# Optimization experiments

Measured on AMD Instinct MI355X. Metric: run time of the kernel, lower is better.

Reference implementation:

```python
import jax, jax.numpy as jnp
import numpy as np

N_NODES = 50000
N_EDGES = 600000
F_IN = 128   # nfeature
H = 128      # nhidden (must equal nfeature due to original code's gcn2 init)
C = 10       # nclass


def setup_inputs() -> dict:
    key = jax.random.key(0)
    ks = jax.random.split(key, 8)
    row = jax.random.randint(ks[0], (N_EDGES,), 0, N_NODES)
    col = jax.random.randint(ks[1], (N_EDGES,), 0, N_NODES)
    label = jax.random.randint(ks[2], (N_EDGES,), 0, C)
    features = jax.random.normal(ks[3], (N_NODES, F_IN), dtype=jnp.float32)
    s1 = 1.0 / np.sqrt(F_IN)
    W1 = jax.random.uniform(ks[4], (H, F_IN), jnp.float32, -s1, s1)
    b1 = jnp.zeros((H,), jnp.float32)
    s2 = 1.0 / np.sqrt(H)
    W2 = jax.random.uniform(ks[5], (H, H), jnp.float32, -s2, s2)
    b2 = jnp.zeros((H,), jnp.float32)
    s3 = 1.0 / np.sqrt(2 * H)
    Wfc = jax.random.uniform(ks[6], (C, 2 * H), jnp.float32, -s3, s3)
    bfc = jnp.zeros((C,), jnp.float32)
    return {"features": features, "W1": W1, "b1": b1, "W2": W2, "b2": b2,
            "Wfc": Wfc, "bfc": bfc, "row": row, "col": col, "label": label}


def gcn_conv(x, row, col, W, b):
    # GCNConv: add self loops, linear, then deg-normalized scatter-add.
    n = x.shape[0]
    sl = jnp.arange(n, dtype=row.dtype)
    r = jnp.concatenate([row, sl])  # source / j index (PyG edge_index[0])
    c = jnp.concatenate([col, sl])  # target / aggregation index (edge_index[1])
    h = x @ W.T + b  # [N, H]
    # degree computed over row of self-loop-augmented edge_index (>=1 always)
    deg = jax.ops.segment_sum(jnp.ones(r.shape, h.dtype), r, num_segments=n)
    dinv = deg ** -0.5
    norm = dinv[r] * dinv[c]  # [E+N]
    msg = norm[:, None] * h[r]  # gather + scale, [E+N, H]
    return jax.ops.segment_sum(msg, c, num_segments=n)  # scatter-add, [N, H]


def reference(features, W1, b1, W2, b2, Wfc, bfc, row, col, label):
    h1 = gcn_conv(features, row, col, W1, b1)  # [N, H]
    h2 = gcn_conv(h1, row, col, W2, b2)        # [N, H]
    # take_logits: index_select per edge endpoint, concat on feature dim
    x = jnp.concatenate([h2[row], h2[col]], axis=1)  # [E, 2H]
    logits = x @ Wfc.T + bfc  # [E, C]
    logp = jax.nn.log_softmax(logits, axis=-1)
    loss = -jnp.mean(jnp.take_along_axis(logp, label[:, None], axis=1))
    return loss, logits
```

## Files before the change

### kernel.cpp

```cpp
#include <hip/hip_runtime.h>
#include <hip/hip_bf16.h>
#include <math.h>

#define NND 50000
#define NE  600000
#define HD  128
#define NC  10
#define CAP 64
#define NCH 64
#define ECHUNK 9375
#define HBIN8 25000
#define SCB 128
#define HISTB 256
#define GEMMB 782
#define LOSSB 2344

typedef unsigned short ushort_t;
typedef unsigned char uchar_t;
typedef __attribute__((ext_vector_type(8))) short short8;
typedef __attribute__((ext_vector_type(4))) float f32x4;

__device__ __forceinline__ float bf2f(unsigned short u) {
  return __uint_as_float(((unsigned int)u) << 16);
}
__device__ __forceinline__ unsigned short f2bf(float f) {
  __hip_bfloat16 h = __float2bfloat16(f);
  return *(unsigned short*)&h;
}

__global__ __launch_bounds__(256) void k_hist_prep(const int* __restrict__ row,
                                                   const int* __restrict__ col,
                                                   uchar_t* __restrict__ partC,
                                                   uchar_t* __restrict__ partR,
                                                   const float* __restrict__ Wfc,
                                                   const float* __restrict__ W1,
                                                   const float* __restrict__ W2,
                                                   ushort_t* __restrict__ Bp,
                                                   ushort_t* __restrict__ Bw1,
                                                   ushort_t* __restrict__ Bw2) {
  __shared__ unsigned int h32[HBIN8 / 4];
  int bb = blockIdx.x, tid = threadIdx.x;
  if (bb < HISTB) {
    const int* src = (bb < SCB) ? col : row;
    uchar_t* dst = (bb < SCB) ? partC : partR;
    int hb = bb & (SCB - 1);
    int cb = hb & 63, half = hb >> 6;
    int binbase = half * HBIN8;
    for (int i = tid; i < HBIN8 / 4; i += 256) h32[i] = 0;
    __syncthreads();
    int e0 = cb * ECHUNK;
    for (int e = e0 + tid; e < e0 + ECHUNK; e += 256) {
      int r = src[e] - binbase;
      if (r >= 0 && r < HBIN8)
        atomicAdd(&h32[r >> 2], 1u << ((r & 3) * 8));
    }
    __syncthreads();
    unsigned int* d32 = (unsigned int*)(dst + (size_t)hb * HBIN8);
    for (int i = tid; i < HBIN8 / 4; i += 256) d32[i] = h32[i];
  } else if (bb == HISTB) {
    for (int idx = tid; idx < 8 * 64; idx += 256) {
      int t = idx >> 6, lane = idx & 63;
      int n = lane & 15, q = (lane >> 4) & 3;
      #pragma unroll
      for (int j = 0; j < 8; j++) {
        int k = t * 32 + q * 8 + j;
        float v = (n < NC) ? Wfc[n * 256 + k] : 0.f;
        Bp[idx * 8 + j] = f2bf(v);
      }
    }
  } else {
    int pb = bb - HISTB - 1;
    const float* W = (pb < 8) ? W1 : W2;
    ushort_t* B = (pb < 8) ? Bw1 : Bw2;
    int nt = pb & 7;
    for (int idx = tid; idx < 4 * 64; idx += 256) {
      int t = idx >> 6, lane = idx & 63;
      int n = nt * 16 + (lane & 15), q = (lane >> 4) & 3;
      #pragma unroll
      for (int j = 0; j < 8; j++) {
        int k = t * 32 + q * 8 + j;
        B[(nt * 256 + idx) * 8 + j] = f2bf(W[n * HD + k]);
      }
    }
  }
}

__global__ __launch_bounds__(256) void k_off(const uchar_t* __restrict__ partC,
                                             const uchar_t* __restrict__ partR,
                                             uchar_t* __restrict__ off8,
                                             int* __restrict__ pos,
                                             float* __restrict__ dinv,
                                             float* __restrict__ out) {
  if (blockIdx.x == 0 && threadIdx.x == 0) out[0] = 0.f;
  int n = blockIdx.x * 256 + threadIdx.x;
  if (n >= NND) return;
  int half = (n >= HBIN8) ? 1 : 0;
  int local = n - half * HBIN8;
  int run = 0;
  #pragma unroll 8
  for (int cb = 0; cb < NCH; cb++) {
    int v = partC[(size_t)(half * NCH + cb) * HBIN8 + local];
    off8[(size_t)cb * NND + n] = (uchar_t)run;
    run += v;
  }
  pos[n] = run;
  int rs = 0;
  #pragma unroll 8
  for (int cb = 0; cb < NCH; cb++) rs += partR[(size_t)(half * NCH + cb) * HBIN8 + local];
  dinv[n] = rsqrtf(1.0f + (float)rs);
}

template <bool FP32IN>
__device__ __forceinline__ void gemm_body(const void* __restrict__ Xv,
                                          const ushort_t* __restrict__ Bw,
                                          const float* __restrict__ b,
                                          ushort_t* __restrict__ Y,
                                          ushort_t* Bs, int bid, int tid) {
  for (int i = tid; i < 2048; i += 256)
    *(short8*)&Bs[i * 8] = *(const short8*)&Bw[i * 8];
  __syncthreads();
  int w = tid >> 6, lane = tid & 63;
  int m = lane & 15, q = lane >> 4;
  int rowbase = bid * 64 + w * 16;
  int rm = rowbase + m; if (rm >= NND) rm = NND - 1;
  short8 a[4];
  if (FP32IN) {
    const float* X = (const float*)Xv;
    #pragma unroll
    for (int t = 0; t < 4; t++) {
      const float* p0 = &X[(long)rm * HD + t * 32 + q * 8];
      float4 x0 = *(const float4*)p0;
      float4 x1 = *(const float4*)(p0 + 4);
      short8 av;
      av[0] = (short)f2bf(x0.x); av[1] = (short)f2bf(x0.y);
      av[2] = (short)f2bf(x0.z); av[3] = (short)f2bf(x0.w);
      av[4] = (short)f2bf(x1.x); av[5] = (short)f2bf(x1.y);
      av[6] = (short)f2bf(x1.z); av[7] = (short)f2bf(x1.w);
      a[t] = av;
    }
  } else {
    const ushort_t* X = (const ushort_t*)Xv;
    #pragma unroll
    for (int t = 0; t < 4; t++)
      a[t] = *(const short8*)&X[(long)rm * HD + t * 32 + q * 8];
  }
  #pragma unroll
  for (int nt = 0; nt < 8; nt++) {
    f32x4 acc = {0.f, 0.f, 0.f, 0.f};
    #pragma unroll
    for (int t = 0; t < 4; t++) {
      short8 bf = *(const short8*)&Bs[((nt * 4 + t) * 64 + lane) * 8];
      acc = __builtin_amdgcn_mfma_f32_16x16x32_bf16(a[t], bf, acc, 0, 0, 0);
    }
    float bias = b[nt * 16 + m];
    #pragma unroll
    for (int reg = 0; reg < 4; reg++) {
      int r = rowbase + q * 4 + reg;
      if (r < NND) Y[(long)r * HD + nt * 16 + m] = f2bf(acc[reg] + bias);
    }
  }
}

__global__ __launch_bounds__(256) void k_mega(const float* __restrict__ features,
                                              const ushort_t* __restrict__ Bw1,
                                              const float* __restrict__ b1,
                                              ushort_t* __restrict__ Y,
                                              const int* __restrict__ row,
                                              const int* __restrict__ col,
                                              const uchar_t* __restrict__ off8,
                                              int* __restrict__ srcs) {
  __shared__ ushort_t smem[16384];
  int tid = threadIdx.x;
  int bb = blockIdx.x;
  if (bb < SCB) {
    unsigned int* h32 = (unsigned int*)smem;
    int cb = bb & 63, half = bb >> 6;
    int binbase = half * HBIN8;
    for (int i = tid; i < HBIN8 / 4; i += 256) h32[i] = 0;
    __syncthreads();
    int e0 = cb * ECHUNK;
    const uchar_t* offc = &off8[(size_t)cb * NND];
    for (int e = e0 + tid; e < e0 + ECHUNK; e += 256) {
      int c = col[e];
      int r = c - binbase;
      if (r >= 0 && r < HBIN8) {
        unsigned int old = atomicAdd(&h32[r >> 2], 1u << ((r & 3) * 8));
        int loc = (old >> ((r & 3) * 8)) & 0xff;
        int p = offc[c] + loc;
        if (p < CAP) srcs[(size_t)c * CAP + p] = row[e];
      }
    }
  } else {
    gemm_body<true>((const void*)features, Bw1, b1, Y, smem, bb - SCB, tid);
  }
}

__global__ __launch_bounds__(256) void k_aggr(const ushort_t* __restrict__ H,
                                              const int* __restrict__ srcs,
                                              const int* __restrict__ pos,
                                              const float* __restrict__ dinv,
                                              ushort_t* __restrict__ O) {
  int g = threadIdx.x >> 5, lane = threadIdx.x & 31;
  int half = lane >> 4;
  int fl = (lane & 15) * 8;
  int node = blockIdx.x * 8 + g;
  if (node >= NND) return;
  float di = dinv[node];
  short8 hv = *(const short8*)&H[(long)node * HD + fl];
  float acc[8];
  float sw = (half == 0) ? di * di : 0.0f;
  #pragma unroll
  for (int j = 0; j < 8; j++) acc[j] = sw * bf2f((unsigned short)hv[j]);
  int cnt = pos[node]; if (cnt > CAP) cnt = CAP;
  const int* nb = &srcs[(long)node * CAP];
  for (int base = 0; base < cnt; base += 32) {
    int m = cnt - base; if (m > 32) m = 32;
    int sl = 0; float wl = 0.f;
    if (lane < m) { sl = nb[base + lane]; wl = di * dinv[sl]; }
    int iters = (m + 1) >> 1;
    int u = 0;
    for (; u + 1 < iters; u += 2) {
      int t0 = 2 * u + half, t1 = t0 + 2;
      int s0 = __shfl(sl, t0 & 31, 32); float w0 = __shfl(wl, t0 & 31, 32);
      int s1 = __shfl(sl, t1 & 31, 32); float w1 = __shfl(wl, t1 & 31, 32);
      short8 h0 = *(const short8*)&H[(long)s0 * HD + fl];
      short8 h1 = *(const short8*)&H[(long)s1 * HD + fl];
      #pragma unroll
      for (int j = 0; j < 8; j++) acc[j] += w0 * bf2f((unsigned short)h0[j]);
      #pragma unroll
      for (int j = 0; j < 8; j++) acc[j] += w1 * bf2f((unsigned short)h1[j]);
    }
    if (u < iters) {
      int t = 2 * u + half;
      int s = __shfl(sl, t & 31, 32); float w = __shfl(wl, t & 31, 32);
      short8 hs = *(const short8*)&H[(long)s * HD + fl];
      #pragma unroll
      for (int j = 0; j < 8; j++) acc[j] += w * bf2f((unsigned short)hs[j]);
    }
  }
  #pragma unroll
  for (int j = 0; j < 8; j++) acc[j] += __shfl(acc[j], (lane & 15) + 16, 32);
  if (half == 0) {
    short8 r;
    #pragma unroll
    for (int j = 0; j < 8; j++) r[j] = (short)f2bf(acc[j]);
    *(short8*)&O[(long)node * HD + fl] = r;
  }
}

__global__ __launch_bounds__(256) void k_gemm2q(const ushort_t* __restrict__ X,
                                                const ushort_t* __restrict__ Bw,
                                                const float* __restrict__ b,
                                                const ushort_t* __restrict__ Bp,
                                                ushort_t* __restrict__ Q) {
  __shared__ ushort_t Bs[16384];
  __shared__ ushort_t Ts[4 * 16 * 136];
  int tid = threadIdx.x;
  for (int i = tid; i < 2048; i += 256)
    *(short8*)&Bs[i * 8] = *(const short8*)&Bw[i * 8];
  __syncthreads();
  int w = tid >> 6, lane = tid & 63;
  int m = lane & 15, q = lane >> 4;
  int rowbase = blockIdx.x * 64 + w * 16;
  int rm = rowbase + m; if (rm >= NND) rm = NND - 1;
  short8 a[4];
  #pragma unroll
  for (int t = 0; t < 4; t++)
    a[t] = *(const short8*)&X[(long)rm * HD + t * 32 + q * 8];
  ushort_t* Tw = &Ts[w * 2176];
  #pragma unroll
  for (int nt = 0; nt < 8; nt++) {
    f32x4 acc = {0.f, 0.f, 0.f, 0.f};
    #pragma unroll
    for (int t = 0; t < 4; t++) {
      short8 bf = *(const short8*)&Bs[((nt * 4 + t) * 64 + lane) * 8];
      acc = __builtin_amdgcn_mfma_f32_16x16x32_bf16(a[t], bf, acc, 0, 0, 0);
    }
    float bias = b[nt * 16 + m];
    #pragma unroll
    for (int reg = 0; reg < 4; reg++)
      Tw[(q * 4 + reg) * 136 + nt * 16 + m] = f2bf(acc[reg] + bias);
  }
  short8 a2[4];
  #pragma unroll
  for (int t = 0; t < 4; t++)
    a2[t] = *(const short8*)&Tw[m * 136 + t * 32 + q * 8];
  f32x4 aL = {0.f, 0.f, 0.f, 0.f}, aR = {0.f, 0.f, 0.f, 0.f};
  #pragma unroll
  for (int t = 0; t < 4; t++) {
    short8 bl = *(const short8*)&Bp[(t * 64 + lane) * 8];
    short8 br = *(const short8*)&Bp[((4 + t) * 64 + lane) * 8];
    aL = __builtin_amdgcn_mfma_f32_16x16x32_bf16(a2[t], bl, aL, 0, 0, 0);
    aR = __builtin_amdgcn_mfma_f32_16x16x32_bf16(a2[t], br, aR, 0, 0, 0);
  }
  if (m < 12) {
    #pragma unroll
    for (int reg = 0; reg < 4; reg++) {
      int r = rowbase + q * 4 + reg;
      if (r < NND) {
        Q[(long)r * 24 + m]      = f2bf(aL[reg]);
        Q[(long)r * 24 + 12 + m] = f2bf(aR[reg]);
      }
    }
  }
}

__global__ __launch_bounds__(256) void k_aggr2(const ushort_t* __restrict__ Q,
                                               const int* __restrict__ srcs,
                                               const int* __restrict__ pos,
                                               const float* __restrict__ dinv,
                                               float* __restrict__ Pr,
                                               float* __restrict__ Pc) {
  int g = threadIdx.x >> 5, lane = threadIdx.x & 31;
  int half = lane >> 4;
  int f = lane & 15;
  int node = blockIdx.x * 8 + g;
  if (node >= NND) return;
  float di = dinv[node];
  bool act = (f < 12);
  unsigned int qv = act ? *(const unsigned int*)&Q[(long)node * 24 + 2 * f] : 0u;
  float sw = (half == 0) ? di * di : 0.f;
  float a0 = sw * bf2f((ushort_t)(qv & 0xffff));
  float a1 = sw * bf2f((ushort_t)(qv >> 16));
  int cnt = pos[node]; if (cnt > CAP) cnt = CAP;
  const int* nb = &srcs[(long)node * CAP];
  for (int base = 0; base < cnt; base += 32) {
    int m2 = cnt - base; if (m2 > 32) m2 = 32;
    int sl = 0; float wl = 0.f;
    if (lane < m2) { sl = nb[base + lane]; wl = di * dinv[sl]; }
    int iters = (m2 + 1) >> 1;
    int u = 0;
    for (; u + 1 < iters; u += 2) {
      int t0 = 2 * u + half, t1 = t0 + 2;
      int s0 = __shfl(sl, t0 & 31, 32); float w0 = __shfl(wl, t0 & 31, 32);
      int s1 = __shfl(sl, t1 & 31, 32); float w1 = __shfl(wl, t1 & 31, 32);
      unsigned int h0 = act ? *(const unsigned int*)&Q[(long)s0 * 24 + 2 * f] : 0u;
      unsigned int h1 = act ? *(const unsigned int*)&Q[(long)s1 * 24 + 2 * f] : 0u;
      a0 += w0 * bf2f((ushort_t)(h0 & 0xffff));
      a1 += w0 * bf2f((ushort_t)(h0 >> 16));
      a0 += w1 * bf2f((ushort_t)(h1 & 0xffff));
      a1 += w1 * bf2f((ushort_t)(h1 >> 16));
    }
    if (u < iters) {
      int t = 2 * u + half;
      int s = __shfl(sl, t & 31, 32); float wv = __shfl(wl, t & 31, 32);
      unsigned int hs = act ? *(const unsigned int*)&Q[(long)s * 24 + 2 * f] : 0u;
      a0 += wv * bf2f((ushort_t)(hs & 0xffff));
      a1 += wv * bf2f((ushort_t)(hs >> 16));
    }
  }
  a0 += __shfl(a0, f + 16, 32);
  a1 += __shfl(a1, f + 16, 32);
  if (half == 0 && act) {
    float2 v; v.x = a0; v.y = a1;
    if (f < 6) *(float2*)&Pr[(long)node * 12 + 2 * f] = v;
    else       *(float2*)&Pc[(long)node * 12 + 2 * (f - 6)] = v;
  }
}

__global__ __launch_bounds__(256) void k_edge(const float* __restrict__ Pr,
                                              const float* __restrict__ Pc,
                                              const int* __restrict__ row,
                                              const int* __restrict__ col,
                                              const int* __restrict__ label,
                                              const float* __restrict__ bfc,
                                              float* __restrict__ logits,
                                              float* __restrict__ out) {
  __shared__ __align__(16) float S[2560];
  __shared__ float Ls[4];
  int tid = threadIdx.x;
  long e0 = (long)blockIdx.x * 256;
  int e = (int)e0 + tid;
  float lp = 0.f;
  if (e < NE) {
    int r = row[e], c = col[e];
    const float* pr = &Pr[(long)r * 12];
    const float* pc = &Pc[(long)c * 12];
    float4 r0 = *(const float4*)&pr[0];
    float4 r1 = *(const float4*)&pr[4];
    float4 r2 = *(const float4*)&pr[8];
    float4 c0 = *(const float4*)&pc[0];
    float4 c1 = *(const float4*)&pc[4];
    float4 c2 = *(const float4*)&pc[8];
    float p[NC];
    p[0] = r0.x + c0.x + bfc[0]; p[1] = r0.y + c0.y + bfc[1];
    p[2] = r0.z + c0.z + bfc[2]; p[3] = r0.w + c0.w + bfc[3];
    p[4] = r1.x + c1.x + bfc[4]; p[5] = r1.y + c1.y + bfc[5];
    p[6] = r1.z + c1.z + bfc[6]; p[7] = r1.w + c1.w + bfc[7];
    p[8] = r2.x + c2.x + bfc[8]; p[9] = r2.y + c2.y + bfc[9];
    #pragma unroll
    for (int cc = 0; cc < NC; cc++) S[tid * 10 + cc] = p[cc];
    float mx = p[0];
    #pragma unroll
    for (int cc = 1; cc < NC; cc++) mx = fmaxf(mx, p[cc]);
    float se = 0.f;
    #pragma unroll
    for (int cc = 0; cc < NC; cc++) se += __expf(p[cc] - mx);
    int lb = label[e];
    float plb = p[0];
    #pragma unroll
    for (int cc = 1; cc < NC; cc++) plb = (cc == lb) ? p[cc] : plb;
    lp = plb - mx - __logf(se);
  }
  __syncthreads();
  int ve = NE - (int)e0; if (ve > 256) ve = 256;
  int limF4 = ve * 10 / 4;
  float4* dst = (float4*)&logits[e0 * 10];
  const float4* src4 = (const float4*)S;
  for (int i = tid; i < limF4; i += 256) dst[i] = src4[i];
  #pragma unroll
  for (int off = 32; off > 0; off >>= 1) lp += __shfl_xor(lp, off, 64);
  if ((tid & 63) == 0) Ls[tid >> 6] = lp;
  __syncthreads();
  if (tid == 0)
    atomicAdd(out, -(Ls[0] + Ls[1] + Ls[2] + Ls[3]) / (float)NE);
}

extern "C" void kernel_launch(void* const* d_in, const int* in_sizes, int n_in,
                              void* d_out, int out_size, void* d_ws, size_t ws_size,
                              hipStream_t stream) {
  const float* features = (const float*)d_in[0];
  const float* W1  = (const float*)d_in[1];
  const float* b1  = (const float*)d_in[2];
  const float* W2  = (const float*)d_in[3];
  const float* b2  = (const float*)d_in[4];
  const float* Wfc = (const float*)d_in[5];
  const float* bfc = (const float*)d_in[6];
  const int* row   = (const int*)d_in[7];
  const int* col   = (const int*)d_in[8];
  const int* label = (const int*)d_in[9];
  float* out = (float*)d_out;

  float* ws = (float*)d_ws;
  size_t o = 0;
  int*   pos      = (int*)(ws + o);     o += 50048;
  int*   srcs     = (int*)(ws + o);     o += (size_t)NND * CAP;
  uchar_t* partC  = (uchar_t*)(ws + o); o += SCB * HBIN8 / 4;
  uchar_t* partR  = (uchar_t*)(ws + o); o += SCB * HBIN8 / 4;
  uchar_t* off8   = (uchar_t*)(ws + o); o += NCH * NND / 4;
  float* dinv     = ws + o;             o += 50048;
  float* partial  = ws + o;             o += LOSSB + 8;
  float* Pr       = ws + o;             o += (size_t)NND * 12;
  float* Pc       = ws + o;             o += (size_t)NND * 12;
  ushort_t* Bp  = (ushort_t*)(ws + o);  o += 2048;
  ushort_t* Bw1 = (ushort_t*)(ws + o);  o += 8192;
  ushort_t* Bw2 = (ushort_t*)(ws + o);  o += 8192;
  ushort_t* bufA = (ushort_t*)(ws + o); o += 3200000;
  ushort_t* bufB = (ushort_t*)(ws + o); o += 3200000;
  (void)partial;
  ushort_t* Q = bufA;

  k_hist_prep<<<HISTB + 17, 256, 0, stream>>>(row, col, partC, partR,
                                              Wfc, W1, W2, Bp, Bw1, Bw2);
  k_off<<<196, 256, 0, stream>>>(partC, partR, off8, pos, dinv, out);
  k_mega<<<SCB + GEMMB, 256, 0, stream>>>(features, Bw1, b1, bufA, row, col, off8, srcs);
  k_aggr<<<6250, 256, 0, stream>>>(bufA, srcs, pos, dinv, bufB);
  k_gemm2q<<<GEMMB, 256, 0, stream>>>(bufB, Bw2, b2, Bp, Q);
  k_aggr2<<<6250, 256, 0, stream>>>(Q, srcs, pos, dinv, Pr, Pc);
  k_edge<<<LOSSB, 256, 0, stream>>>(Pr, Pc, row, col, label, bfc, out + 1, out);
}
```

Measured before the change: 237.6 us.

## Replace deterministic histogram CSR build with global-atomic bucketing and inline weight conversion

Drops the histogram and prefix-offset kernels (partitioned byte histograms plus an offset pass) and builds the per-node source lists with global atomicAdd on pos and deg inside the fused front kernel, which also runs the first GEMM. Weight conversion to bf16 MFMA layout now happens inside each GEMM block instead of a separate prep pass, and dinv is recomputed from integer degrees on the fly. This cuts two launches and several full passes over the edge arrays, at the cost of global atomic contention, a memset, and neighbour order that now depends on scheduling, so float summation order varies between runs.

```diff
diff --git a/kernel.cpp b/kernel.cpp
--- a/kernel.cpp
+++ b/kernel.cpp
@@ -7,11 +7,7 @@
 #define HD  128
 #define NC  10
 #define CAP 64
-#define NCH 64
-#define ECHUNK 9375
-#define HBIN8 25000
-#define SCB 128
-#define HISTB 256
+#define SCATB 256
 #define GEMMB 782
 #define LOSSB 2344
 
@@ -28,96 +24,29 @@
   return *(unsigned short*)&h;
 }
 
-__global__ __launch_bounds__(256) void k_hist_prep(const int* __restrict__ row,
-                                                   const int* __restrict__ col,
-                                                   uchar_t* __restrict__ partC,
-                                                   uchar_t* __restrict__ partR,
-                                                   const float* __restrict__ Wfc,
-                                                   const float* __restrict__ W1,
-                                                   const float* __restrict__ W2,
-                                                   ushort_t* __restrict__ Bp,
-                                                   ushort_t* __restrict__ Bw1,
-                                                   ushort_t* __restrict__ Bw2) {
-  __shared__ unsigned int h32[HBIN8 / 4];
-  int bb = blockIdx.x, tid = threadIdx.x;
-  if (bb < HISTB) {
-    const int* src = (bb < SCB) ? col : row;
-    uchar_t* dst = (bb < SCB) ? partC : partR;
-    int hb = bb & (SCB - 1);
-    int cb = hb & 63, half = hb >> 6;
-    int binbase = half * HBIN8;
-    for (int i = tid; i < HBIN8 / 4; i += 256) h32[i] = 0;
-    __syncthreads();
-    int e0 = cb * ECHUNK;
-    for (int e = e0 + tid; e < e0 + ECHUNK; e += 256) {
-      int r = src[e] - binbase;
-      if (r >= 0 && r < HBIN8)
-        atomicAdd(&h32[r >> 2], 1u << ((r & 3) * 8));
-    }
-    __syncthreads();
-    unsigned int* d32 = (unsigned int*)(dst + (size_t)hb * HBIN8);
-    for (int i = tid; i < HBIN8 / 4; i += 256) d32[i] = h32[i];
-  } else if (bb == HISTB) {
-    for (int idx = tid; idx < 8 * 64; idx += 256) {
-      int t = idx >> 6, lane = idx & 63;
-      int n = lane & 15, q = (lane >> 4) & 3;
-      #pragma unroll
-      for (int j = 0; j < 8; j++) {
-        int k = t * 32 + q * 8 + j;
-        float v = (n < NC) ? Wfc[n * 256 + k] : 0.f;
-        Bp[idx * 8 + j] = f2bf(v);
-      }
-    }
-  } else {
-    int pb = bb - HISTB - 1;
-    const float* W = (pb < 8) ? W1 : W2;
-    ushort_t* B = (pb < 8) ? Bw1 : Bw2;
-    int nt = pb & 7;
-    for (int idx = tid; idx < 4 * 64; idx += 256) {
-      int t = idx >> 6, lane = idx & 63;
-      int n = nt * 16 + (lane & 15), q = (lane >> 4) & 3;
-      #pragma unroll
-      for (int j = 0; j < 8; j++) {
-        int k = t * 32 + q * 8 + j;
-        B[(nt * 256 + idx) * 8 + j] = f2bf(W[n * HD + k]);
-      }
-    }
-  }
-}
-
-__global__ __launch_bounds__(256) void k_off(const uchar_t* __restrict__ partC,
-                                             const uchar_t* __restrict__ partR,
-                                             uchar_t* __restrict__ off8,
-                                             int* __restrict__ pos,
-                                             float* __restrict__ dinv,
-                                             float* __restrict__ out) {
-  if (blockIdx.x == 0 && threadIdx.x == 0) out[0] = 0.f;
-  int n = blockIdx.x * 256 + threadIdx.x;
-  if (n >= NND) return;
-  int half = (n >= HBIN8) ? 1 : 0;
-  int local = n - half * HBIN8;
-  int run = 0;
-  #pragma unroll 8
-  for (int cb = 0; cb < NCH; cb++) {
-    int v = partC[(size_t)(half * NCH + cb) * HBIN8 + local];
-    off8[(size_t)cb * NND + n] = (uchar_t)run;
-    run += v;
-  }
-  pos[n] = run;
-  int rs = 0;
-  #pragma unroll 8
-  for (int cb = 0; cb < NCH; cb++) rs += partR[(size_t)(half * NCH + cb) * HBIN8 + local];
-  dinv[n] = rsqrtf(1.0f + (float)rs);
+__device__ __forceinline__ short8 f2bf8(const float* __restrict__ p) {
+  float4 x0 = *(const float4*)p;
+  float4 x1 = *(const float4*)(p + 4);
+  short8 v;
+  v[0] = (short)f2bf(x0.x); v[1] = (short)f2bf(x0.y);
+  v[2] = (short)f2bf(x0.z); v[3] = (short)f2bf(x0.w);
+  v[4] = (short)f2bf(x1.x); v[5] = (short)f2bf(x1.y);
+  v[6] = (short)f2bf(x1.z); v[7] = (short)f2bf(x1.w);
+  return v;
 }
 
 template <bool FP32IN>
-__device__ __forceinline__ void gemm_body(const void* __restrict__ Xv,
-                                          const ushort_t* __restrict__ Bw,
-                                          const float* __restrict__ b,
-                                          ushort_t* __restrict__ Y,
-                                          ushort_t* Bs, int bid, int tid) {
-  for (int i = tid; i < 2048; i += 256)
-    *(short8*)&Bs[i * 8] = *(const short8*)&Bw[i * 8];
+__device__ __forceinline__ void gemm_body_w(const void* __restrict__ Xv,
+                                            const float* __restrict__ W,
+                                            const float* __restrict__ b,
+                                            ushort_t* __restrict__ Y,
+                                            ushort_t* Bs, int bid, int tid) {
+  for (int idx = tid; idx < 2048; idx += 256) {
+    int g = idx >> 6, lane = idx & 63;
+    int nt = g >> 2, t = g & 3;
+    int n = nt * 16 + (lane & 15), q = (lane >> 4) & 3;
+    *(short8*)&Bs[idx * 8] = f2bf8(&W[n * HD + t * 32 + q * 8]);
+  }
   __syncthreads();
   int w = tid >> 6, lane = tid & 63;
   int m = lane & 15, q = lane >> 4;
@@ -127,17 +56,8 @@
   if (FP32IN) {
     const float* X = (const float*)Xv;
     #pragma unroll
-    for (int t = 0; t < 4; t++) {
-      const float* p0 = &X[(long)rm * HD + t * 32 + q * 8];
-      float4 x0 = *(const float4*)p0;
-      float4 x1 = *(const float4*)(p0 + 4);
-      short8 av;
-      av[0] = (short)f2bf(x0.x); av[1] = (short)f2bf(x0.y);
-      av[2] = (short)f2bf(x0.z); av[3] = (short)f2bf(x0.w);
-      av[4] = (short)f2bf(x1.x); av[5] = (short)f2bf(x1.y);
-      av[6] = (short)f2bf(x1.z); av[7] = (short)f2bf(x1.w);
-      a[t] = av;
-    }
+    for (int t = 0; t < 4; t++)
+      a[t] = f2bf8(&X[(long)rm * HD + t * 32 + q * 8]);
   } else {
     const ushort_t* X = (const ushort_t*)Xv;
     #pragma unroll
@@ -161,51 +81,43 @@
   }
 }
 
-__global__ __launch_bounds__(256) void k_mega(const float* __restrict__ features,
-                                              const ushort_t* __restrict__ Bw1,
-                                              const float* __restrict__ b1,
-                                              ushort_t* __restrict__ Y,
-                                              const int* __restrict__ row,
-                                              const int* __restrict__ col,
-                                              const uchar_t* __restrict__ off8,
-                                              int* __restrict__ srcs) {
-  __shared__ ushort_t smem[16384];
-  int tid = threadIdx.x;
-  int bb = blockIdx.x;
-  if (bb < SCB) {
-    unsigned int* h32 = (unsigned int*)smem;
-    int cb = bb & 63, half = bb >> 6;
-    int binbase = half * HBIN8;
-    for (int i = tid; i < HBIN8 / 4; i += 256) h32[i] = 0;
-    __syncthreads();
-    int e0 = cb * ECHUNK;
-    const uchar_t* offc = &off8[(size_t)cb * NND];
-    for (int e = e0 + tid; e < e0 + ECHUNK; e += 256) {
-      int c = col[e];
-      int r = c - binbase;
-      if (r >= 0 && r < HBIN8) {
-        unsigned int old = atomicAdd(&h32[r >> 2], 1u << ((r & 3) * 8));
-        int loc = (old >> ((r & 3) * 8)) & 0xff;
-        int p = offc[c] + loc;
-        if (p < CAP) srcs[(size_t)c * CAP + p] = row[e];
-      }
+__global__ __launch_bounds__(256) void k_front(const int* __restrict__ row,
+                                               const int* __restrict__ col,
+                                               int* __restrict__ pos,
+                                               int* __restrict__ deg,
+                                               int* __restrict__ srcs,
+                                               const float* __restrict__ features,
+                                               const float* __restrict__ W1,
+                                               const float* __restrict__ b1,
+                                               ushort_t* __restrict__ Y,
+                                               float* __restrict__ out) {
+  __shared__ ushort_t Bs[16384];
+  int tid = threadIdx.x, bb = blockIdx.x;
+  if (bb < SCATB) {
+    if (bb == 0 && tid == 0) out[0] = 0.f;
+    int stride = SCATB * 256;
+    for (int e = bb * 256 + tid; e < NE; e += stride) {
+      int c = col[e], r = row[e];
+      int slot = atomicAdd(&pos[c], 1);
+      if (slot < CAP) srcs[(size_t)c * CAP + slot] = r;
+      atomicAdd(&deg[r], 1);
     }
   } else {
-    gemm_body<true>((const void*)features, Bw1, b1, Y, smem, bb - SCB, tid);
+    gemm_body_w<true>((const void*)features, W1, b1, Y, Bs, bb - SCATB, tid);
   }
 }
 
 __global__ __launch_bounds__(256) void k_aggr(const ushort_t* __restrict__ H,
                                               const int* __restrict__ srcs,
                                               const int* __restrict__ pos,
-                                              const float* __restrict__ dinv,
+                                              const int* __restrict__ deg,
                                               ushort_t* __restrict__ O) {
   int g = threadIdx.x >> 5, lane = threadIdx.x & 31;
   int half = lane >> 4;
   int fl = (lane & 15) * 8;
   int node = blockIdx.x * 8 + g;
   if (node >= NND) return;
-  float di = dinv[node];
+  float di = rsqrtf(1.0f + (float)deg[node]);
   short8 hv = *(const short8*)&H[(long)node * HD + fl];
   float acc[8];
   float sw = (half == 0) ? di * di : 0.0f;
@@ -216,7 +128,7 @@
   for (int base = 0; base < cnt; base += 32) {
     int m = cnt - base; if (m > 32) m = 32;
     int sl = 0; float wl = 0.f;
-    if (lane < m) { sl = nb[base + lane]; wl = di * dinv[sl]; }
+    if (lane < m) { sl = nb[base + lane]; wl = di * rsqrtf(1.0f + (float)deg[sl]); }
     int iters = (m + 1) >> 1;
     int u = 0;
     for (; u + 1 < iters; u += 2) {
@@ -249,15 +161,19 @@
 }
 
 __global__ __launch_bounds__(256) void k_gemm2q(const ushort_t* __restrict__ X,
-                                                const ushort_t* __restrict__ Bw,
+                                                const float* __restrict__ W2,
                                                 const float* __restrict__ b,
-                                                const ushort_t* __restrict__ Bp,
+                                                const float* __restrict__ Wfc,
                                                 ushort_t* __restrict__ Q) {
   __shared__ ushort_t Bs[16384];
   __shared__ ushort_t Ts[4 * 16 * 136];
   int tid = threadIdx.x;
-  for (int i = tid; i < 2048; i += 256)
-    *(short8*)&Bs[i * 8] = *(const short8*)&Bw[i * 8];
+  for (int idx = tid; idx < 2048; idx += 256) {
+    int g = idx >> 6, lane2 = idx & 63;
+    int nt = g >> 2, t = g & 3;
+    int n2 = nt * 16 + (lane2 & 15), q2 = (lane2 >> 4) & 3;
+    *(short8*)&Bs[idx * 8] = f2bf8(&W2[n2 * HD + t * 32 + q2 * 8]);
+  }
   __syncthreads();
   int w = tid >> 6, lane = tid & 63;
   int m = lane & 15, q = lane >> 4;
@@ -287,11 +203,11 @@
     a2[t] = *(const short8*)&Tw[m * 136 + t * 32 + q * 8];
   f32x4 aL = {0.f, 0.f, 0.f, 0.f}, aR = {0.f, 0.f, 0.f, 0.f};
   #pragma unroll
-  for (int t = 0; t < 4; t++) {
-    short8 bl = *(const short8*)&Bp[(t * 64 + lane) * 8];
-    short8 br = *(const short8*)&Bp[((4 + t) * 64 + lane) * 8];
-    aL = __builtin_amdgcn_mfma_f32_16x16x32_bf16(a2[t], bl, aL, 0, 0, 0);
-    aR = __builtin_amdgcn_mfma_f32_16x16x32_bf16(a2[t], br, aR, 0, 0, 0);
+  for (int t = 0; t < 8; t++) {
+    short8 bv = {0, 0, 0, 0, 0, 0, 0, 0};
+    if (m < NC) bv = f2bf8(&Wfc[m * 256 + t * 32 + q * 8]);
+    if (t < 4) aL = __builtin_amdgcn_mfma_f32_16x16x32_bf16(a2[t], bv, aL, 0, 0, 0);
+    else       aR = __builtin_amdgcn_mfma_f32_16x16x32_bf16(a2[t & 3], bv, aR, 0, 0, 0);
   }
   if (m < 12) {
     #pragma unroll
@@ -308,7 +224,7 @@
 __global__ __launch_bounds__(256) void k_aggr2(const ushort_t* __restrict__ Q,
                                                const int* __restrict__ srcs,
                                                const int* __restrict__ pos,
-                                               const float* __restrict__ dinv,
+                                               const int* __restrict__ deg,
                                                float* __restrict__ Pr,
                                                float* __restrict__ Pc) {
   int g = threadIdx.x >> 5, lane = threadIdx.x & 31;
@@ -316,7 +232,7 @@
   int f = lane & 15;
   int node = blockIdx.x * 8 + g;
   if (node >= NND) return;
-  float di = dinv[node];
+  float di = rsqrtf(1.0f + (float)deg[node]);
   bool act = (f < 12);
   unsigned int qv = act ? *(const unsigned int*)&Q[(long)node * 24 + 2 * f] : 0u;
   float sw = (half == 0) ? di * di : 0.f;
@@ -327,7 +243,7 @@
   for (int base = 0; base < cnt; base += 32) {
     int m2 = cnt - base; if (m2 > 32) m2 = 32;
     int sl = 0; float wl = 0.f;
-    if (lane < m2) { sl = nb[base + lane]; wl = di * dinv[sl]; }
+    if (lane < m2) { sl = nb[base + lane]; wl = di * rsqrtf(1.0f + (float)deg[sl]); }
     int iters = (m2 + 1) >> 1;
     int u = 0;
     for (; u + 1 < iters; u += 2) {
@@ -431,31 +347,20 @@
   const int* label = (const int*)d_in[9];
   float* out = (float*)d_out;
 
-  float* ws = (float*)d_ws;
-  size_t o = 0;
-  int*   pos      = (int*)(ws + o);     o += 50048;
-  int*   srcs     = (int*)(ws + o);     o += (size_t)NND * CAP;
-  uchar_t* partC  = (uchar_t*)(ws + o); o += SCB * HBIN8 / 4;
-  uchar_t* partR  = (uchar_t*)(ws + o); o += SCB * HBIN8 / 4;
-  uchar_t* off8   = (uchar_t*)(ws + o); o += NCH * NND / 4;
-  float* dinv     = ws + o;             o += 50048;
-  float* partial  = ws + o;             o += LOSSB + 8;
-  float* Pr       = ws + o;             o += (size_t)NND * 12;
-  float* Pc       = ws + o;             o += (size_t)NND * 12;
-  ushort_t* Bp  = (ushort_t*)(ws + o);  o += 2048;
-  ushort_t* Bw1 = (ushort_t*)(ws + o);  o += 8192;
-  ushort_t* Bw2 = (ushort_t*)(ws + o);  o += 8192;
-  ushort_t* bufA = (ushort_t*)(ws + o); o += 3200000;
-  ushort_t* bufB = (ushort_t*)(ws + o); o += 3200000;
-  (void)partial;
+  int* pos = (int*)d_ws;
+  int* deg = pos + 50048;
+  int* srcs = deg + 50048;
+  float* Pr = (float*)(srcs + (size_t)NND * CAP);
+  float* Pc = Pr + 600000;
+  ushort_t* bufA = (ushort_t*)(Pc + 600000);
+  ushort_t* bufB = bufA + 6400000;
   ushort_t* Q = bufA;
 
-  k_hist_prep<<<HISTB + 17, 256, 0, stream>>>(row, col, partC, partR,
-                                              Wfc, W1, W2, Bp, Bw1, Bw2);
-  k_off<<<196, 256, 0, stream>>>(partC, partR, off8, pos, dinv, out);
-  k_mega<<<SCB + GEMMB, 256, 0, stream>>>(features, Bw1, b1, bufA, row, col, off8, srcs);
-  k_aggr<<<6250, 256, 0, stream>>>(bufA, srcs, pos, dinv, bufB);
-  k_gemm2q<<<GEMMB, 256, 0, stream>>>(bufB, Bw2, b2, Bp, Q);
-  k_aggr2<<<6250, 256, 0, stream>>>(Q, srcs, pos, dinv, Pr, Pc);
+  hipMemsetAsync(pos, 0, 2 * 50048 * sizeof(int), stream);
+  k_front<<<SCATB + GEMMB, 256, 0, stream>>>(row, col, pos, deg, srcs,
+                                             features, W1, b1, bufA, out);
+  k_aggr<<<6250, 256, 0, stream>>>(bufA, srcs, pos, deg, bufB);
+  k_gemm2q<<<GEMMB, 256, 0, stream>>>(bufB, W2, b2, Wfc, Q);
+  k_aggr2<<<6250, 256, 0, stream>>>(Q, srcs, pos, deg, Pr, Pc);
   k_edge<<<LOSSB, 256, 0, stream>>>(Pr, Pc, row, col, label, bfc, out + 1, out);
 }
```

Measured after the change: 240.5 us. About the same (+1.2%).
